# Performance work log

Measured on AMD Instinct MI355X. Metric: run time of the kernel, lower is better.

The kernel has to match this reference:

```python
import jax, jax.numpy as jnp
import numpy as np

D_MODEL = 2048
HEADS = 16


def setup_inputs() -> dict:
    key = jax.random.key(0)
    ks = jax.random.split(key, 9)
    s = 1.0 / np.sqrt(D_MODEL)
    x = jax.random.normal(ks[0], (2, 2048, D_MODEL), dtype=jnp.float32)
    wq = jax.random.uniform(ks[1], (D_MODEL, D_MODEL), jnp.float32, -s, s)
    wk = jax.random.uniform(ks[2], (D_MODEL, D_MODEL), jnp.float32, -s, s)
    wv = jax.random.uniform(ks[3], (D_MODEL, D_MODEL), jnp.float32, -s, s)
    wo = jax.random.uniform(ks[4], (D_MODEL, D_MODEL), jnp.float32, -s, s)
    bq = jax.random.uniform(ks[5], (D_MODEL,), jnp.float32, -s, s)
    bk = jax.random.uniform(ks[6], (D_MODEL,), jnp.float32, -s, s)
    bv = jax.random.uniform(ks[7], (D_MODEL,), jnp.float32, -s, s)
    bo = jax.random.uniform(ks[8], (D_MODEL,), jnp.float32, -s, s)
    return {"x": x, "wq": wq, "bq": bq, "wk": wk, "bk": bk,
            "wv": wv, "bv": bv, "wo": wo, "bo": bo}


def _split(t, heads):
    b, s, d = t.shape
    return t.reshape(b, s, heads, d // heads).transpose(0, 2, 1, 3)  # [b,h,s,dh]


def reference(x, wq, bq, wk, bk, wv, bv, wo, bo):
    q = x @ wq.T + bq
    k = x @ wk.T + bk
    v = x @ wv.T + bv
    q, k, v = _split(q, HEADS), _split(k, HEADS), _split(v, HEADS)
    dh = q.shape[-1]
    scale = 1.0 / np.sqrt(dh).astype(np.float32)
    score = jnp.einsum('bhqd,bhkd->bhqk', q, k) * scale  # [b,h,s,s]
    score = jax.nn.softmax(score.astype(jnp.float32), axis=-1).astype(q.dtype)
    out = jnp.einsum('bhqk,bhkd->bhqd', score, v)
    b, h, s, _ = out.shape
    out = out.transpose(0, 2, 1, 3).reshape(b, s, h * dh)
    return out @ wo.T + bo
```

## Files before the change

kernel.cpp:

```cpp
#include <hip/hip_runtime.h>
#include <cstdint>
#include <cstddef>

#define D_MODEL 2048
#define SEQ 2048
#define BATCH 2
#define HEADS 16
#define DH 128
#define MROWS (BATCH * SEQ)

typedef __attribute__((ext_vector_type(8))) short short8;
typedef __attribute__((ext_vector_type(4))) float f32x4;
typedef __attribute__((ext_vector_type(16))) float f32x16;
typedef __attribute__((ext_vector_type(2))) unsigned int uint2e;

__device__ __forceinline__ unsigned short f2bf(float f) {
    unsigned int u = __builtin_bit_cast(unsigned int, f);
    u += 0x7fffu + ((u >> 16) & 1u);
    return (unsigned short)(u >> 16);
}

__device__ __forceinline__ unsigned int cvt_pk_bf16(float lo, float hi) {
    unsigned int w;
    asm("v_cvt_pk_bf16_f32 %0, %1, %2" : "=v"(w) : "v"(lo), "v"(hi));
    return w;
}

__device__ __forceinline__ void swap32(unsigned int& x, unsigned int& y) {
#if __has_builtin(__builtin_amdgcn_permlane32_swap)
    uint2e r = __builtin_amdgcn_permlane32_swap(x, y, false, false);
    x = r[0]; y = r[1];
#else
    const int hi = (threadIdx.x >> 5) & 1;
    const unsigned int gx = (unsigned int)__shfl_xor((int)x, 32);
    const unsigned int gy = (unsigned int)__shfl_xor((int)y, 32);
    const unsigned int nx = hi ? gy : x;
    const unsigned int ny = hi ? y : gx;
    x = nx; y = ny;
#endif
}

__device__ __forceinline__ void gload_lds16(const unsigned short* g, unsigned short* l) {
    __builtin_amdgcn_global_load_lds(
        (const __attribute__((address_space(1))) void*)g,
        (__attribute__((address_space(3))) void*)l, 16, 0, 0);
}

__global__ __launch_bounds__(256) void cvt_all(const float* __restrict__ x,
                                               const float* __restrict__ wq,
                                               const float* __restrict__ wk,
                                               const float* __restrict__ wv,
                                               const float* __restrict__ wo,
                                               unsigned short* __restrict__ out) {
    constexpr int PX = (MROWS * D_MODEL) / 4;
    constexpr int PW = (D_MODEL * D_MODEL) / 4;
    int i = blockIdx.x * 256 + threadIdx.x;
    const float* s;
    int off;
    if (i < PX) { s = x; off = i; }
    else {
        const int j = i - PX;
        const int sel = j / PW;
        off = j - sel * PW;
        s = sel == 0 ? wq : sel == 1 ? wk : sel == 2 ? wv : wo;
    }
    const float4 v = reinterpret_cast<const float4*>(s)[off];
    ushort4 o;
    o.x = f2bf(v.x); o.y = f2bf(v.y); o.z = f2bf(v.z); o.w = f2bf(v.w);
    reinterpret_cast<ushort4*>(out)[i] = o;
}

__global__ __launch_bounds__(512, 2)
void gemm3(const unsigned short* __restrict__ X,
           const unsigned short* __restrict__ Wq,
           const unsigned short* __restrict__ Wk,
           const unsigned short* __restrict__ Wv,
           const float* __restrict__ bq,
           const float* __restrict__ bk,
           const float* __restrict__ bv,
           unsigned short* __restrict__ Qb,
           unsigned short* __restrict__ Kb,
           unsigned short* __restrict__ VTb) {
    constexpr int BK = 64;
    constexpr int K = D_MODEL;
    constexpr int NTILES = K / BK;
    constexpr int NWG = 768;
    __shared__ unsigned short As[3][128 * BK];
    __shared__ unsigned short Bs[3][256 * BK];

    const int tid  = threadIdx.x;
    const int lane = tid & 63;
    const int wid  = tid >> 6;

    const int swz = (blockIdx.x & 7) * (NWG >> 3) + (blockIdx.x >> 3);
    const int job   = swz >> 8;
    const int local = swz & 255;

    const unsigned short* aBase;
    const unsigned short* bBase;
    const float* bias;
    unsigned short* cBase;
    int ldc, m0, n0;
    bool brow;
    if (job == 2) {
        m0 = (local >> 4) * 128;
        n0 = (local & 15) * 256;
        aBase = Wv; bBase = X; bias = bv; cBase = VTb; ldc = MROWS; brow = true;
    } else {
        m0 = (local >> 3) * 128;
        n0 = (local & 7) * 256;
        aBase = X;
        bBase = job ? Wk : Wq;
        bias  = job ? bk : bq;
        cBase = job ? Kb : Qb;
        ldc = D_MODEL; brow = false;
    }

    const int srow = tid >> 3;
    const int sch  = tid & 7;
    const int ssw  = (sch ^ (srow & 7)) * 8;
    const int sd   = srow * 64 + sch * 8;
    const unsigned short* aS[2];
#pragma unroll
    for (int j = 0; j < 2; ++j) aS[j] = aBase + (size_t)(m0 + j * 64 + srow) * K + ssw;
    const unsigned short* bS[4];
#pragma unroll
    for (int j = 0; j < 4; ++j) bS[j] = bBase + (size_t)(n0 + j * 64 + srow) * K + ssw;

    const int fr = lane & 15, fg = lane >> 4;
    const int wm = wid >> 2, wn = wid & 3;
    int aoff[4][2], boff[4][2];
#pragma unroll
    for (int i = 0; i < 4; ++i)
#pragma unroll
        for (int ks = 0; ks < 2; ++ks) {
            const int sw = ((ks * 4 + fg) ^ (fr & 7)) * 8;
            aoff[i][ks] = (wm * 64 + i * 16 + fr) * BK + sw;
            boff[i][ks] = (wn * 64 + i * 16 + fr) * BK + sw;
        }

    f32x4 acc[4][4] = {};

    unsigned short *pA0 = As[0], *pA1 = As[1], *pA2 = As[2];
    unsigned short *pB0 = Bs[0], *pB1 = Bs[1], *pB2 = Bs[2];

#define STG_AV(P, T) { _Pragma("unroll") for (int j = 0; j < 2; ++j) \
        gload_lds16(aS[j] + (T) * BK, (P) + j * 4096 + sd); }
#define STG_BV(P, T) { _Pragma("unroll") for (int j = 0; j < 4; ++j) \
        gload_lds16(bS[j] + (T) * BK, (P) + j * 4096 + sd); }

    STG_AV(pA0, 0) STG_BV(pB0, 0)
    STG_AV(pA1, 1) STG_BV(pB1, 1)
    asm volatile("s_waitcnt vmcnt(6)" ::: "memory");
    __builtin_amdgcn_s_barrier();

#pragma unroll 1
    for (int t = 0; t < NTILES; ++t) {
        const bool more = (t + 2 < NTILES);
        short8 aF[4][2], bF0[2][2];
#pragma unroll
        for (int mi = 0; mi < 4; ++mi)
#pragma unroll
            for (int ks = 0; ks < 2; ++ks)
                aF[mi][ks] = *(const short8*)&pA0[aoff[mi][ks]];
#pragma unroll
        for (int ni = 0; ni < 2; ++ni)
#pragma unroll
            for (int ks = 0; ks < 2; ++ks)
                bF0[ni][ks] = *(const short8*)&pB0[boff[ni][ks]];
        if (more) { STG_AV(pA2, t + 2) STG_BV(pB2, t + 2) }
        asm volatile("s_waitcnt lgkmcnt(0)" ::: "memory");
        __builtin_amdgcn_sched_barrier(0);
        __builtin_amdgcn_s_setprio(1);
#pragma unroll
        for (int ks = 0; ks < 2; ++ks)
#pragma unroll
            for (int mi = 0; mi < 4; ++mi)
#pragma unroll
                for (int ni = 0; ni < 2; ++ni)
                    acc[mi][ni] = __builtin_amdgcn_mfma_f32_16x16x32_bf16(
                        aF[mi][ks], bF0[ni][ks], acc[mi][ni], 0, 0, 0);
        __builtin_amdgcn_s_setprio(0);
        short8 bG[2][2];
#pragma unroll
        for (int ni = 0; ni < 2; ++ni)
#pragma unroll
            for (int ks = 0; ks < 2; ++ks)
                bG[ni][ks] = *(const short8*)&pB0[boff[2 + ni][ks]];
        asm volatile("s_waitcnt lgkmcnt(0)" ::: "memory");
        __builtin_amdgcn_sched_barrier(0);
        __builtin_amdgcn_s_setprio(1);
#pragma unroll
        for (int ks = 0; ks < 2; ++ks)
#pragma unroll
            for (int mi = 0; mi < 4; ++mi)
#pragma unroll
                for (int ni = 0; ni < 2; ++ni)
                    acc[mi][2 + ni] = __builtin_amdgcn_mfma_f32_16x16x32_bf16(
                        aF[mi][ks], bG[ni][ks], acc[mi][2 + ni], 0, 0, 0);
        __builtin_amdgcn_s_setprio(0);
        if (more) asm volatile("s_waitcnt vmcnt(6)" ::: "memory");
        else      asm volatile("s_waitcnt vmcnt(0)" ::: "memory");
        __builtin_amdgcn_s_barrier();
        unsigned short* tA = pA0; pA0 = pA1; pA1 = pA2; pA2 = tA;
        unsigned short* tB = pB0; pB0 = pB1; pB1 = pB2; pB2 = tB;
    }
#undef STG_AV
#undef STG_BV

#pragma unroll
    for (int mi = 0; mi < 4; ++mi)
#pragma unroll
        for (int r = 0; r < 4; ++r) {
            const int row = m0 + wm * 64 + mi * 16 + fg * 4 + r;
            const float brv = brow ? bias[row] : 0.f;
#pragma unroll
            for (int ni = 0; ni < 4; ++ni) {
                const int col = n0 + wn * 64 + ni * 16 + fr;
                const float bvv = brow ? brv : bias[col];
                cBase[(size_t)row * ldc + col] = f2bf(acc[mi][ni][r] + bvv);
            }
        }
}

__global__ __launch_bounds__(512, 2)
void gemmT1(const unsigned short* __restrict__ A,
            const unsigned short* __restrict__ W0,
            const float* __restrict__ b0f,
            float* __restrict__ OF) {
    constexpr int BM = 256, BN = 128, BK = 64;
    constexpr int K = D_MODEL;
    constexpr int NTILES = K / BK;
    constexpr int NT_N = 16;
    constexpr int NWG = (MROWS / BM) * NT_N;
    __shared__ unsigned short As[3][BM * BK];
    __shared__ unsigned short Bs[3][BN * BK];

    const int tid  = threadIdx.x;
    const int lane = tid & 63;
    const int wid  = tid >> 6;

    const int wk = (blockIdx.x & 7) * (NWG >> 3) + (blockIdx.x >> 3);
    const int nt = wk % NT_N;
    const int mt = wk / NT_N;
    const int m0 = mt * BM;
    const int n0 = nt * BN;

    const int srow = tid >> 3;
    const int sch  = tid & 7;
    const int ssw  = (sch ^ (srow & 7)) * 8;
    const int sd   = srow * 64 + sch * 8;
    const unsigned short* aS[4];
#pragma unroll
    for (int j = 0; j < 4; ++j) aS[j] = A + (size_t)(m0 + j * 64 + srow) * K + ssw;
    const unsigned short* bS[2];
#pragma unroll
    for (int j = 0; j < 2; ++j) bS[j] = W0 + (size_t)(n0 + j * 64 + srow) * K + ssw;

    const int fr = lane & 15, fg = lane >> 4;
    const int wm = wid >> 1, wn = wid & 1;
    int aoff[4][2], boff[4][2];
#pragma unroll
    for (int mi = 0; mi < 4; ++mi)
#pragma unroll
        for (int ks = 0; ks < 2; ++ks) {
            aoff[mi][ks] = (wm * 64 + mi * 16 + fr) * BK + ((ks * 4 + fg) ^ (fr & 7)) * 8;
            boff[mi][ks] = (wn * 64 + mi * 16 + fr) * BK + ((ks * 4 + fg) ^ (fr & 7)) * 8;
        }

    f32x4 acc[4][4] = {};

    unsigned short *pA0 = As[0], *pA1 = As[1], *pA2 = As[2];
    unsigned short *pB0 = Bs[0], *pB1 = Bs[1], *pB2 = Bs[2];

#define STG_A3(P, T) { _Pragma("unroll") for (int j = 0; j < 4; ++j) \
        gload_lds16(aS[j] + (T) * BK, (P) + j * 4096 + sd); }
#define STG_B3(P, T) { _Pragma("unroll") for (int j = 0; j < 2; ++j) \
        gload_lds16(bS[j] + (T) * BK, (P) + j * 4096 + sd); }

    STG_A3(pA0, 0) STG_B3(pB0, 0)
    STG_A3(pA1, 1) STG_B3(pB1, 1)
    asm volatile("s_waitcnt vmcnt(6)" ::: "memory");
    __builtin_amdgcn_s_barrier();

#pragma unroll 1
    for (int t = 0; t < NTILES; ++t) {
        const bool more = (t + 2 < NTILES);
        short8 aF[4][2], bF0[2][2];
#pragma unroll
        for (int mi = 0; mi < 4; ++mi)
#pragma unroll
            for (int ks = 0; ks < 2; ++ks)
                aF[mi][ks] = *(const short8*)&pA0[aoff[mi][ks]];
#pragma unroll
        for (int ni = 0; ni < 2; ++ni)
#pragma unroll
            for (int ks = 0; ks < 2; ++ks)
                bF0[ni][ks] = *(const short8*)&pB0[boff[ni][ks]];
        if (more) { STG_A3(pA2, t + 2) STG_B3(pB2, t + 2) }
        asm volatile("s_waitcnt lgkmcnt(0)" ::: "memory");
        __builtin_amdgcn_sched_barrier(0);
        __builtin_amdgcn_s_setprio(1);
#pragma unroll
        for (int ks = 0; ks < 2; ++ks)
#pragma unroll
            for (int mi = 0; mi < 4; ++mi)
#pragma unroll
                for (int ni = 0; ni < 2; ++ni)
                    acc[mi][ni] = __builtin_amdgcn_mfma_f32_16x16x32_bf16(
                        aF[mi][ks], bF0[ni][ks], acc[mi][ni], 0, 0, 0);
        __builtin_amdgcn_s_setprio(0);
        short8 bG[2][2];
#pragma unroll
        for (int ni = 0; ni < 2; ++ni)
#pragma unroll
            for (int ks = 0; ks < 2; ++ks)
                bG[ni][ks] = *(const short8*)&pB0[boff[2 + ni][ks]];
        asm volatile("s_waitcnt lgkmcnt(0)" ::: "memory");
        __builtin_amdgcn_sched_barrier(0);
        __builtin_amdgcn_s_setprio(1);
#pragma unroll
        for (int ks = 0; ks < 2; ++ks)
#pragma unroll
            for (int mi = 0; mi < 4; ++mi)
#pragma unroll
                for (int ni = 0; ni < 2; ++ni)
                    acc[mi][2 + ni] = __builtin_amdgcn_mfma_f32_16x16x32_bf16(
                        aF[mi][ks], bG[ni][ks], acc[mi][2 + ni], 0, 0, 0);
        __builtin_amdgcn_s_setprio(0);
        if (more) asm volatile("s_waitcnt vmcnt(6)" ::: "memory");
        else      asm volatile("s_waitcnt vmcnt(0)" ::: "memory");
        __builtin_amdgcn_s_barrier();
        unsigned short* tA = pA0; pA0 = pA1; pA1 = pA2; pA2 = tA;
        unsigned short* tB = pB0; pB0 = pB1; pB1 = pB2; pB2 = tB;
    }
#undef STG_A3
#undef STG_B3

#pragma unroll
    for (int mi = 0; mi < 4; ++mi)
#pragma unroll
        for (int ni = 0; ni < 4; ++ni) {
            const int col = n0 + wn * 64 + ni * 16 + fr;
            const float bv = b0f[col];
#pragma unroll
            for (int r = 0; r < 4; ++r) {
                const int row = m0 + wm * 64 + mi * 16 + fg * 4 + r;
                OF[(size_t)row * D_MODEL + col] = acc[mi][ni][r] + bv;
            }
        }
}

__global__ __launch_bounds__(256, 2)
void flash_attn3(const unsigned short* __restrict__ Q, const unsigned short* __restrict__ Kg,
                 const unsigned short* __restrict__ VT, unsigned short* __restrict__ O) {
    constexpr int KVB = 64;
    constexpr int NT = SEQ / KVB;
    __shared__ unsigned short Ks[2 * KVB * DH];
    __shared__ unsigned short Vs[2 * DH * KVB];

    const int tid  = threadIdx.x;
    const int lane = tid & 63;
    const int wid  = tid >> 6;
    const int l31  = lane & 31;
    const int hi   = lane >> 5;

    const int swz = (blockIdx.x & 7) * 64 + (blockIdx.x >> 3);
    const int qt = swz & 15;
    const int bh = swz >> 4;
    const int b = bh >> 4, h = bh & 15;
    const int qrow = qt * 128 + wid * 32 + l31;

    const unsigned short* Qp = Q + ((size_t)b * SEQ + qrow) * D_MODEL + h * DH;
    const unsigned short* Kp = Kg + (size_t)b * SEQ * D_MODEL + h * DH;
    const unsigned short* Vp = VT + (size_t)(h * DH) * MROWS + (size_t)b * SEQ;

    short8 qf[8];
#pragma unroll
    for (int kk = 0; kk < 8; ++kk)
        qf[kk] = *(const short8*)(Qp + kk * 16 + hi * 8);

    f32x16 acc[4] = {};
    float m_run = -1e30f, l_run = 0.f;
    const float Cc = 0.088388347648318447f * 1.4426950408889634f;
    const float THR = 8.0f / Cc;

    int co[8];
#pragma unroll
    for (int kk = 0; kk < 8; ++kk) co[kk] = ((kk * 2 + hi) ^ (l31 & 7)) * 8;

    int kroff[4], vroff[4];
#pragma unroll
    for (int q = 0; q < 4; ++q) {
        const int row_l = wid * 16 + q * 4 + (lane >> 4);
        kroff[q] = row_l * D_MODEL + ((lane & 15) ^ (row_l & 7)) * 8;
        const int d_l = wid * 32 + q * 8 + (lane >> 3);
        vroff[q] = d_l * MROWS + ((lane & 7) ^ (d_l & 7)) * 8;
    }
    unsigned short* KsW = Ks + (wid * 16) * DH;
    unsigned short* VsW = Vs + (wid * 32) * KVB;

#pragma unroll
    for (int q = 0; q < 4; ++q) {
        gload_lds16(Kp + kroff[q], KsW + q * 4 * DH);
        gload_lds16(Vp + vroff[q], VsW + q * 8 * KVB);
    }
    __syncthreads();

#pragma unroll 1
    for (int t = 0; t < NT; ++t) {
        const int cur = t & 1;
        if (t + 1 < NT) {
            const unsigned short* Kt = Kp + (size_t)((t + 1) * KVB) * D_MODEL;
            const unsigned short* Vt = Vp + (t + 1) * KVB;
            unsigned short* kd = KsW + (cur ^ 1) * (KVB * DH);
            unsigned short* vd = VsW + (cur ^ 1) * (DH * KVB);
#pragma unroll
            for (int q = 0; q < 4; ++q) {
                gload_lds16(Kt + kroff[q], kd + q * 4 * DH);
                gload_lds16(Vt + vroff[q], vd + q * 8 * KVB);
            }
        }
        const unsigned short* Kc = Ks + cur * (KVB * DH);
        const unsigned short* Vc = Vs + cur * (DH * KVB);

        f32x16 st0 = {}, st1 = {};
        __builtin_amdgcn_s_setprio(1);
#pragma unroll
        for (int kk = 0; kk < 8; ++kk) {
            const short8 kf0 = *(const short8*)&Kc[l31 * DH + co[kk]];
            const short8 kf1 = *(const short8*)&Kc[(32 + l31) * DH + co[kk]];
            st0 = __builtin_amdgcn_mfma_f32_32x32x16_bf16(kf0, qf[kk], st0, 0, 0, 0);
            st1 = __builtin_amdgcn_mfma_f32_32x32x16_bf16(kf1, qf[kk], st1, 0, 0, 0);
        }
        __builtin_amdgcn_s_setprio(0);

        float lm = -1e30f;
#pragma unroll
        for (int r = 0; r < 16; ++r) lm = fmaxf(lm, fmaxf(st0[r], st1[r]));
        {
            unsigned int a = __builtin_bit_cast(unsigned int, lm), bb = a;
            swap32(a, bb);
            lm = fmaxf(lm, __builtin_bit_cast(float, hi ? a : bb));
        }
        if (__any(lm > m_run + THR)) {
            const float mn = fmaxf(m_run, lm);
            const float sf = __builtin_amdgcn_exp2f((m_run - mn) * Cc);
            m_run = mn;
            l_run *= sf;
#pragma unroll
            for (int db = 0; db < 4; ++db)
#pragma unroll
                for (int r = 0; r < 16; ++r) acc[db][r] *= sf;
        }
        const float mc = m_run * Cc;
        float p0[16], p1[16];
        float ps = 0.f;
#pragma unroll
        for (int r = 0; r < 16; ++r) {
            p0[r] = __builtin_amdgcn_exp2f(__builtin_fmaf(st0[r], Cc, -mc));
            p1[r] = __builtin_amdgcn_exp2f(__builtin_fmaf(st1[r], Cc, -mc));
            ps += p0[r] + p1[r];
        }
        {
            unsigned int a = __builtin_bit_cast(unsigned int, ps), bb = a;
            swap32(a, bb);
            ps += __builtin_bit_cast(float, hi ? a : bb);
        }
        l_run += ps;

        unsigned int W0[8], W1[8];
#pragma unroll
        for (int tt = 0; tt < 8; ++tt) {
            W0[tt] = cvt_pk_bf16(p0[2 * tt], p0[2 * tt + 1]);
            W1[tt] = cvt_pk_bf16(p1[2 * tt], p1[2 * tt + 1]);
        }
        swap32(W0[0], W0[2]); swap32(W0[1], W0[3]);
        swap32(W0[4], W0[6]); swap32(W0[5], W0[7]);
        swap32(W1[0], W1[2]); swap32(W1[1], W1[3]);
        swap32(W1[4], W1[6]); swap32(W1[5], W1[7]);
        short8 pf[4];
        {
            uint4 f;
            f.x = W0[0]; f.y = W0[1]; f.z = W0[2]; f.w = W0[3];
            pf[0] = __builtin_bit_cast(short8, f);
            f.x = W0[4]; f.y = W0[5]; f.z = W0[6]; f.w = W0[7];
            pf[1] = __builtin_bit_cast(short8, f);
            f.x = W1[0]; f.y = W1[1]; f.z = W1[2]; f.w = W1[3];
            pf[2] = __builtin_bit_cast(short8, f);
            f.x = W1[4]; f.y = W1[5]; f.z = W1[6]; f.w = W1[7];
            pf[3] = __builtin_bit_cast(short8, f);
        }

        __builtin_amdgcn_s_setprio(1);
#pragma unroll
        for (int db = 0; db < 4; ++db) {
#pragma unroll
            for (int kk16 = 0; kk16 < 4; ++kk16) {
                const short8 vf = *(const short8*)&Vc[(db * 32 + l31) * KVB + co[kk16]];
                acc[db] = __builtin_amdgcn_mfma_f32_32x32x16_bf16(vf, pf[kk16], acc[db], 0, 0, 0);
            }
        }
        __builtin_amdgcn_s_setprio(0);
        __syncthreads();
    }

    const float inv_l = 1.0f / l_run;
    unsigned short* Op = O + ((size_t)b * SEQ + qrow) * D_MODEL + h * DH;
#pragma unroll
    for (int db = 0; db < 4; ++db)
#pragma unroll
        for (int g = 0; g < 4; ++g) {
            ushort4 o4;
            o4.x = f2bf(acc[db][4 * g + 0] * inv_l);
            o4.y = f2bf(acc[db][4 * g + 1] * inv_l);
            o4.z = f2bf(acc[db][4 * g + 2] * inv_l);
            o4.w = f2bf(acc[db][4 * g + 3] * inv_l);
            *(ushort4*)(Op + db * 32 + g * 8 + hi * 4) = o4;
        }
}

extern "C" void kernel_launch(void* const* d_in, const int* in_sizes, int n_in,
                              void* d_out, int out_size, void* d_ws, size_t ws_size,
                              hipStream_t stream) {
    (void)in_sizes; (void)n_in; (void)out_size; (void)ws_size;
    const float* x  = (const float*)d_in[0];
    const float* wq = (const float*)d_in[1];
    const float* bq = (const float*)d_in[2];
    const float* wk = (const float*)d_in[3];
    const float* bk = (const float*)d_in[4];
    const float* wv = (const float*)d_in[5];
    const float* bv = (const float*)d_in[6];
    const float* wo = (const float*)d_in[7];
    const float* bo = (const float*)d_in[8];
    float* out = (float*)d_out;

    unsigned short* ws = (unsigned short*)d_ws;
    const size_t NX = (size_t)MROWS * D_MODEL;
    const size_t NW = (size_t)D_MODEL * D_MODEL;
    unsigned short* xb  = ws;
    unsigned short* wqb = xb + NX;
    unsigned short* wkb = wqb + NW;
    unsigned short* wvb = wkb + NW;
    unsigned short* wob = wvb + NW;
    unsigned short* Qb  = wob + NW;
    unsigned short* Kb  = Qb + NX;
    unsigned short* VTb = Kb + NX;
    unsigned short* Ab  = VTb + NX;

    const unsigned cvt_blocks = (unsigned)((NX + 4 * NW) / 1024);
    cvt_all<<<cvt_blocks, 256, 0, stream>>>(x, wq, wk, wv, wo, xb);

    gemm3<<<768, 512, 0, stream>>>(xb, wqb, wkb, wvb, bq, bk, bv, Qb, Kb, VTb);

    flash_attn3<<<512, 256, 0, stream>>>(Qb, Kb, VTb, Ab);

    gemmT1<<<256, 512, 0, stream>>>(Ab, wob, bo, out);
}
```

Baseline: 271.9 us.

## Split fused QKV GEMM into templated per-projection launches and reuse for output GEMM

Replaces the single 768-block fused QKV kernel with a templated GEMM instantiated per projection (three 256-block launches), removing runtime job selection and per-element bias branching. The output projection now uses the same 128x256 tile kernel in float-output mode instead of the dedicated 256x128 kernel. This specialises the code paths and may cut register pressure, but adds launch overhead and leaves each QKV launch with only 256 blocks, which can underfill the GPU and lose the tail overlap the fused launch provided.

New measurement: 252.1 us. -7.3%, faster.

```diff
diff --git a/kernel.cpp b/kernel.cpp
--- a/kernel.cpp
+++ b/kernel.cpp
@@ -70,21 +70,17 @@
     reinterpret_cast<ushort4*>(out)[i] = o;
 }
 
+template <int MODE>
 __global__ __launch_bounds__(512, 2)
-void gemm3(const unsigned short* __restrict__ X,
-           const unsigned short* __restrict__ Wq,
-           const unsigned short* __restrict__ Wk,
-           const unsigned short* __restrict__ Wv,
-           const float* __restrict__ bq,
-           const float* __restrict__ bk,
-           const float* __restrict__ bv,
-           unsigned short* __restrict__ Qb,
-           unsigned short* __restrict__ Kb,
-           unsigned short* __restrict__ VTb) {
+void gemmU(const unsigned short* __restrict__ Abase,
+           const unsigned short* __restrict__ Bbase,
+           const float* __restrict__ bias,
+           unsigned short* __restrict__ Cb,
+           float* __restrict__ Cf) {
     constexpr int BK = 64;
     constexpr int K = D_MODEL;
     constexpr int NTILES = K / BK;
-    constexpr int NWG = 768;
+    constexpr int NWG = 256;
     __shared__ unsigned short As[3][128 * BK];
     __shared__ unsigned short Bs[3][256 * BK];
 
@@ -93,28 +89,10 @@
     const int wid  = tid >> 6;
 
     const int swz = (blockIdx.x & 7) * (NWG >> 3) + (blockIdx.x >> 3);
-    const int job   = swz >> 8;
-    const int local = swz & 255;
-
-    const unsigned short* aBase;
-    const unsigned short* bBase;
-    const float* bias;
-    unsigned short* cBase;
-    int ldc, m0, n0;
-    bool brow;
-    if (job == 2) {
-        m0 = (local >> 4) * 128;
-        n0 = (local & 15) * 256;
-        aBase = Wv; bBase = X; bias = bv; cBase = VTb; ldc = MROWS; brow = true;
-    } else {
-        m0 = (local >> 3) * 128;
-        n0 = (local & 7) * 256;
-        aBase = X;
-        bBase = job ? Wk : Wq;
-        bias  = job ? bk : bq;
-        cBase = job ? Kb : Qb;
-        ldc = D_MODEL; brow = false;
-    }
+    int m0, n0;
+    if constexpr (MODE == 1) { m0 = (swz >> 4) * 128; n0 = (swz & 15) * 256; }
+    else                     { m0 = (swz >> 3) * 128; n0 = (swz & 7) * 256; }
+    constexpr int LDC = (MODE == 1) ? MROWS : D_MODEL;
 
     const int srow = tid >> 3;
     const int sch  = tid & 7;
@@ -122,10 +100,10 @@
     const int sd   = srow * 64 + sch * 8;
     const unsigned short* aS[2];
 #pragma unroll
-    for (int j = 0; j < 2; ++j) aS[j] = aBase + (size_t)(m0 + j * 64 + srow) * K + ssw;
+    for (int j = 0; j < 2; ++j) aS[j] = Abase + (size_t)(m0 + j * 64 + srow) * K + ssw;
     const unsigned short* bS[4];
 #pragma unroll
-    for (int j = 0; j < 4; ++j) bS[j] = bBase + (size_t)(n0 + j * 64 + srow) * K + ssw;
+    for (int j = 0; j < 4; ++j) bS[j] = Bbase + (size_t)(n0 + j * 64 + srow) * K + ssw;
 
     const int fr = lane & 15, fg = lane >> 4;
     const int wm = wid >> 2, wn = wid & 3;
@@ -213,140 +191,16 @@
 #pragma unroll
         for (int r = 0; r < 4; ++r) {
             const int row = m0 + wm * 64 + mi * 16 + fg * 4 + r;
-            const float brv = brow ? bias[row] : 0.f;
+            const float brv = (MODE == 1) ? bias[row] : 0.f;
 #pragma unroll
             for (int ni = 0; ni < 4; ++ni) {
                 const int col = n0 + wn * 64 + ni * 16 + fr;
-                const float bvv = brow ? brv : bias[col];
-                cBase[(size_t)row * ldc + col] = f2bf(acc[mi][ni][r] + bvv);
-            }
-        }
-}
-
-__global__ __launch_bounds__(512, 2)
-void gemmT1(const unsigned short* __restrict__ A,
-            const unsigned short* __restrict__ W0,
-            const float* __restrict__ b0f,
-            float* __restrict__ OF) {
-    constexpr int BM = 256, BN = 128, BK = 64;
-    constexpr int K = D_MODEL;
-    constexpr int NTILES = K / BK;
-    constexpr int NT_N = 16;
-    constexpr int NWG = (MROWS / BM) * NT_N;
-    __shared__ unsigned short As[3][BM * BK];
-    __shared__ unsigned short Bs[3][BN * BK];
-
-    const int tid  = threadIdx.x;
-    const int lane = tid & 63;
-    const int wid  = tid >> 6;
-
-    const int wk = (blockIdx.x & 7) * (NWG >> 3) + (blockIdx.x >> 3);
-    const int nt = wk % NT_N;
-    const int mt = wk / NT_N;
-    const int m0 = mt * BM;
-    const int n0 = nt * BN;
-
-    const int srow = tid >> 3;
-    const int sch  = tid & 7;
-    const int ssw  = (sch ^ (srow & 7)) * 8;
-    const int sd   = srow * 64 + sch * 8;
-    const unsigned short* aS[4];
-#pragma unroll
-    for (int j = 0; j < 4; ++j) aS[j] = A + (size_t)(m0 + j * 64 + srow) * K + ssw;
-    const unsigned short* bS[2];
-#pragma unroll
-    for (int j = 0; j < 2; ++j) bS[j] = W0 + (size_t)(n0 + j * 64 + srow) * K + ssw;
-
-    const int fr = lane & 15, fg = lane >> 4;
-    const int wm = wid >> 1, wn = wid & 1;
-    int aoff[4][2], boff[4][2];
-#pragma unroll
-    for (int mi = 0; mi < 4; ++mi)
-#pragma unroll
-        for (int ks = 0; ks < 2; ++ks) {
-            aoff[mi][ks] = (wm * 64 + mi * 16 + fr) * BK + ((ks * 4 + fg) ^ (fr & 7)) * 8;
-            boff[mi][ks] = (wn * 64 + mi * 16 + fr) * BK + ((ks * 4 + fg) ^ (fr & 7)) * 8;
-        }
-
-    f32x4 acc[4][4] = {};
-
-    unsigned short *pA0 = As[0], *pA1 = As[1], *pA2 = As[2];
-    unsigned short *pB0 = Bs[0], *pB1 = Bs[1], *pB2 = Bs[2];
-
-#define STG_A3(P, T) { _Pragma("unroll") for (int j = 0; j < 4; ++j) \
-        gload_lds16(aS[j] + (T) * BK, (P) + j * 4096 + sd); }
-#define STG_B3(P, T) { _Pragma("unroll") for (int j = 0; j < 2; ++j) \
-        gload_lds16(bS[j] + (T) * BK, (P) + j * 4096 + sd); }
-
-    STG_A3(pA0, 0) STG_B3(pB0, 0)
-    STG_A3(pA1, 1) STG_B3(pB1, 1)
-    asm volatile("s_waitcnt vmcnt(6)" ::: "memory");
-    __builtin_amdgcn_s_barrier();
-
-#pragma unroll 1
-    for (int t = 0; t < NTILES; ++t) {
-        const bool more = (t + 2 < NTILES);
-        short8 aF[4][2], bF0[2][2];
-#pragma unroll
-        for (int mi = 0; mi < 4; ++mi)
-#pragma unroll
-            for (int ks = 0; ks < 2; ++ks)
-                aF[mi][ks] = *(const short8*)&pA0[aoff[mi][ks]];
-#pragma unroll
-        for (int ni = 0; ni < 2; ++ni)
-#pragma unroll
-            for (int ks = 0; ks < 2; ++ks)
-                bF0[ni][ks] = *(const short8*)&pB0[boff[ni][ks]];
-        if (more) { STG_A3(pA2, t + 2) STG_B3(pB2, t + 2) }
-        asm volatile("s_waitcnt lgkmcnt(0)" ::: "memory");
-        __builtin_amdgcn_sched_barrier(0);
-        __builtin_amdgcn_s_setprio(1);
-#pragma unroll
-        for (int ks = 0; ks < 2; ++ks)
-#pragma unroll
-            for (int mi = 0; mi < 4; ++mi)
-#pragma unroll
-                for (int ni = 0; ni < 2; ++ni)
-                    acc[mi][ni] = __builtin_amdgcn_mfma_f32_16x16x32_bf16(
-                        aF[mi][ks], bF0[ni][ks], acc[mi][ni], 0, 0, 0);
-        __builtin_amdgcn_s_setprio(0);
-        short8 bG[2][2];
-#pragma unroll
-        for (int ni = 0; ni < 2; ++ni)
-#pragma unroll
-            for (int ks = 0; ks < 2; ++ks)
-                bG[ni][ks] = *(const short8*)&pB0[boff[2 + ni][ks]];
-        asm volatile("s_waitcnt lgkmcnt(0)" ::: "memory");
-        __builtin_amdgcn_sched_barrier(0);
-        __builtin_amdgcn_s_setprio(1);
-#pragma unroll
-        for (int ks = 0; ks < 2; ++ks)
-#pragma unroll
-            for (int mi = 0; mi < 4; ++mi)
-#pragma unroll
-                for (int ni = 0; ni < 2; ++ni)
-                    acc[mi][2 + ni] = __builtin_amdgcn_mfma_f32_16x16x32_bf16(
-                        aF[mi][ks], bG[ni][ks], acc[mi][2 + ni], 0, 0, 0);
-        __builtin_amdgcn_s_setprio(0);
-        if (more) asm volatile("s_waitcnt vmcnt(6)" ::: "memory");
-        else      asm volatile("s_waitcnt vmcnt(0)" ::: "memory");
-        __builtin_amdgcn_s_barrier();
-        unsigned short* tA = pA0; pA0 = pA1; pA1 = pA2; pA2 = tA;
-        unsigned short* tB = pB0; pB0 = pB1; pB1 = pB2; pB2 = tB;
-    }
-#undef STG_A3
-#undef STG_B3
-
-#pragma unroll
-    for (int mi = 0; mi < 4; ++mi)
-#pragma unroll
-        for (int ni = 0; ni < 4; ++ni) {
-            const int col = n0 + wn * 64 + ni * 16 + fr;
-            const float bv = b0f[col];
-#pragma unroll
-            for (int r = 0; r < 4; ++r) {
-                const int row = m0 + wm * 64 + mi * 16 + fg * 4 + r;
-                OF[(size_t)row * D_MODEL + col] = acc[mi][ni][r] + bv;
+                const float v = acc[mi][ni][r] + ((MODE == 1) ? brv : bias[col]);
+                if constexpr (MODE == 2) {
+                    Cf[(size_t)row * LDC + col] = v;
+                } else {
+                    Cb[(size_t)row * LDC + col] = f2bf(v);
+                }
             }
         }
 }
@@ -551,9 +405,11 @@
     const unsigned cvt_blocks = (unsigned)((NX + 4 * NW) / 1024);
     cvt_all<<<cvt_blocks, 256, 0, stream>>>(x, wq, wk, wv, wo, xb);
 
-    gemm3<<<768, 512, 0, stream>>>(xb, wqb, wkb, wvb, bq, bk, bv, Qb, Kb, VTb);
+    gemmU<0><<<256, 512, 0, stream>>>(xb, wqb, bq, Qb, nullptr);
+    gemmU<0><<<256, 512, 0, stream>>>(xb, wkb, bk, Kb, nullptr);
+    gemmU<1><<<256, 512, 0, stream>>>(wvb, xb, bv, VTb, nullptr);
 
     flash_attn3<<<512, 256, 0, stream>>>(Qb, Kb, VTb, Ab);
 
-    gemmT1<<<256, 512, 0, stream>>>(Ab, wob, bo, out);
-}
+    gemmU<2><<<256, 512, 0, stream>>>(Ab, wob, bo, nullptr, out);
+}
```
